# Kernel optimization log

Measured on AMD Instinct MI355X. Metric: run time of the kernel, lower is better.

The kernel has to match this reference:

```python
import jax, jax.numpy as jnp
import numpy as np

NEG_SLOPE = 0.2

def gat_conv(x, src, dst, W, a_src, a_dst, bias, num_nodes, heads, out_ch, concat):
    # x: [N, Fin]; W: [Fin, heads*out_ch]; a_src/a_dst: [heads, out_ch]
    h = (x @ W).reshape(num_nodes, heads, out_ch)            # [N,H,C]
    alpha_s = jnp.einsum('nhc,hc->nh', h, a_src)             # [N,H]
    alpha_d = jnp.einsum('nhc,hc->nh', h, a_dst)             # [N,H]
    e = alpha_s[src] + alpha_d[dst]                          # [E,H]
    e = jnp.where(e > 0, e, NEG_SLOPE * e)                   # LeakyReLU
    # segment softmax over incoming edges per destination node
    m = jax.ops.segment_max(e, dst, num_segments=num_nodes)  # [N,H]
    m = jnp.where(jnp.isfinite(m), m, 0.0)
    ee = jnp.exp(e - m[dst])                                 # [E,H]
    s = jax.ops.segment_sum(ee, dst, num_segments=num_nodes) # [N,H]
    alpha = ee / (s[dst] + 1e-16)                            # [E,H]
    out = jax.ops.segment_sum(h[src] * alpha[:, :, None], dst,
                              num_segments=num_nodes)        # [N,H,C]
    if concat:
        out = out.reshape(num_nodes, heads * out_ch)
    else:
        out = out.mean(axis=1)
    return out + bias


def setup_inputs() -> dict:
    key = jax.random.key(0)
    ks = jax.random.split(key, 10)
    N, E = 50000, 800000
    EMB, HID, HEADS, REPR = 128, 128, 8, 64
    C1 = HID // HEADS  # 16
    x = jax.random.normal(ks[0], (N, EMB), dtype=jnp.float32)
    edge_index = jax.random.randint(ks[1], (2, E), 0, N, dtype=jnp.int32)
    sc = 1.0 / np.sqrt(EMB)
    W1 = jax.random.normal(ks[2], (EMB, HEADS * C1), dtype=jnp.float32) * sc
    a1_src = jax.random.normal(ks[3], (HEADS, C1), dtype=jnp.float32) * 0.1
    a1_dst = jax.random.normal(ks[4], (HEADS, C1), dtype=jnp.float32) * 0.1
    b1 = jnp.zeros((HID,), dtype=jnp.float32)
    sc2 = 1.0 / np.sqrt(HID)
    W2 = jax.random.normal(ks[5], (HID, REPR), dtype=jnp.float32) * sc2
    a2_src = jax.random.normal(ks[6], (1, REPR), dtype=jnp.float32) * 0.1
    a2_dst = jax.random.normal(ks[7], (1, REPR), dtype=jnp.float32) * 0.1
    b2 = jnp.zeros((REPR,), dtype=jnp.float32)
    return {"x": x, "edge_index": edge_index,
            "W1": W1, "a1_src": a1_src, "a1_dst": a1_dst, "b1": b1,
            "W2": W2, "a2_src": a2_src, "a2_dst": a2_dst, "b2": b2}


def reference(x, edge_index, W1, a1_src, a1_dst, b1, W2, a2_src, a2_dst, b2):
    N = x.shape[0]
    # PyG GATConv adds self-loops by default
    loops = jnp.arange(N, dtype=edge_index.dtype)
    src = jnp.concatenate([edge_index[0], loops])
    dst = jnp.concatenate([edge_index[1], loops])
    # eval mode: F.dropout(p=0.6) is identity
    h = gat_conv(x, src, dst, W1, a1_src, a1_dst, b1, N,
                 heads=8, out_ch=16, concat=True)
    h = jax.nn.elu(h)
    out = gat_conv(h, src, dst, W2, a2_src, a2_dst, b2, N,
                   heads=1, out_ch=64, concat=True)
    return out
```

## Files before the change

### kernel.cpp

```cpp
#include <hip/hip_runtime.h>
#include <hip/hip_fp16.h>
#include <math.h>


typedef _Float16 f16x8 __attribute__((ext_vector_type(8)));
typedef float f32x4 __attribute__((ext_vector_type(4)));

#define NCHUNK 32
#define MAXBDIV 8192

__device__ __forceinline__ float leaky_exp(float e) {
    e = (e > 0.f) ? e : 0.2f * e;
    return __expf(e);
}

__device__ __forceinline__ void acc16(float w, float4 hv0, float4 hv1,
                                      float* __restrict__ acc) {
    const __half2* p0 = (const __half2*)&hv0;
    const __half2* p1 = (const __half2*)&hv1;
#pragma unroll
    for (int k = 0; k < 4; k++) {
        float2 f = __half22float2(p0[k]);
        acc[2 * k] += w * f.x;
        acc[2 * k + 1] += w * f.y;
    }
#pragma unroll
    for (int k = 0; k < 4; k++) {
        float2 f = __half22float2(p1[k]);
        acc[8 + 2 * k] += w * f.x;
        acc[8 + 2 * k + 1] += w * f.y;
    }
}

__device__ __forceinline__ void acc8(float w, float4 hv,
                                     float* __restrict__ acc) {
    const __half2* hp = (const __half2*)&hv;
#pragma unroll
    for (int k = 0; k < 4; k++) {
        float2 f = __half22float2(hp[k]);
        acc[2 * k] += w * f.x;
        acc[2 * k + 1] += w * f.y;
    }
}

__global__ __launch_bounds__(256) void augw_kernel(const float* __restrict__ W1,
                                                   const float* __restrict__ a1s,
                                                   const float* __restrict__ a1d,
                                                   const float* __restrict__ W2,
                                                   const float* __restrict__ a2s,
                                                   const float* __restrict__ a2d,
                                                   _Float16* __restrict__ W1t,
                                                   _Float16* __restrict__ W2t) {
    int t = threadIdx.x;
    if (blockIdx.x == 0) {
        for (int i = t; i < 144 * 128; i += 256) {
            int c = i >> 7, k = i & 127;
            float v;
            if (c < 128) {
                v = W1[k * 128 + c];
            } else if (c < 136) {
                int h = c - 128; v = 0.f;
#pragma unroll
                for (int j = 0; j < 16; j++) v += W1[k * 128 + h * 16 + j] * a1s[h * 16 + j];
            } else {
                int h = c - 136; v = 0.f;
#pragma unroll
                for (int j = 0; j < 16; j++) v += W1[k * 128 + h * 16 + j] * a1d[h * 16 + j];
            }
            W1t[c * 128 + k] = (_Float16)v;
        }
    } else {
        for (int i = t; i < 80 * 128; i += 256) {
            int c = i >> 7, k = i & 127;
            float v = 0.f;
            if (c < 64) {
                v = W2[k * 64 + c];
            } else if (c == 64) {
                for (int j = 0; j < 64; j++) v += W2[k * 64 + j] * a2s[j];
            } else if (c == 65) {
                for (int j = 0; j < 64; j++) v += W2[k * 64 + j] * a2d[j];
            }
            W2t[c * 128 + k] = (_Float16)v;
        }
    }
}

__global__ __launch_bounds__(256) void gemm1_bucket_kernel(
        const float* __restrict__ x, const _Float16* __restrict__ W1t,
        __half* __restrict__ h1, float* __restrict__ als,
        float* __restrict__ ald, int N, int gridG1,
        const int* __restrict__ src, const int* __restrict__ dst, int E,
        int* __restrict__ bucketCnt, int2* __restrict__ pairs) {
    __shared__ _Float16 Xs[64 * 136];
    int t = threadIdx.x;
    if ((int)blockIdx.x >= gridG1) {
        int* lcnt = (int*)Xs;
        int* lbase = lcnt + 8;
        if (t < 8) lcnt[t] = 0;
        __syncthreads();
        int bid = blockIdx.x - gridG1;
        int bdiv = (N + 7) >> 3;
        int i0 = (bid * 256 + t) * 4;
        int s_[4], d_[4], bk[4], rk[4];
        int nv = 0;
        if (i0 + 3 < E) {
            int4 d4 = *(const int4*)(dst + i0);
            int4 s4 = *(const int4*)(src + i0);
            s_[0] = s4.x; s_[1] = s4.y; s_[2] = s4.z; s_[3] = s4.w;
            d_[0] = d4.x; d_[1] = d4.y; d_[2] = d4.z; d_[3] = d4.w;
            nv = 4;
        } else {
            for (int k = i0; k < E && nv < 4; k++) {
                s_[nv] = src[k]; d_[nv] = dst[k]; nv++;
            }
        }
        int lane = t & 63;
        unsigned long long below = (lane == 0) ? 0ULL : (~0ULL >> (64 - lane));
#pragma unroll
        for (int u = 0; u < 4; u++) {
            bool v = (u < nv);
            int d = v ? d_[u] : 0;
            int b = d / bdiv;
            unsigned long long m0 = __ballot(b & 1);
            unsigned long long m1 = __ballot(b & 2);
            unsigned long long m2 = __ballot(b & 4);
            unsigned long long vm = __ballot(v);
            unsigned long long me = ((b & 1) ? m0 : ~m0) & ((b & 2) ? m1 : ~m1) &
                                    ((b & 4) ? m2 : ~m2) & vm;
            int leader = __ffsll((unsigned long long)me) - 1;
            int ldr = (leader < 0) ? 0 : leader;
            int cnt = __popcll(me);
            int rank = __popcll(me & below);
            int base = 0;
            if (v && lane == leader) base = atomicAdd(&lcnt[b], cnt);
            base = __shfl(base, ldr);
            bk[u] = b;
            rk[u] = base + rank;
        }
        __syncthreads();
        if (t < 8) lbase[t] = atomicAdd(&bucketCnt[t * 16], lcnt[t]);
        __syncthreads();
#pragma unroll 4
        for (int k = 0; k < nv; k++) {
            pairs[(size_t)bk[k] * E + lbase[bk[k]] + rk[k]] = make_int2(s_[k], d_[k]);
        }
        return;
    }
    int row0 = blockIdx.x * 64;
    for (int i = t; i < 2048; i += 256) {
        int r = i >> 5, c4 = i & 31;
        int gr = row0 + r;
        float4 v = make_float4(0.f, 0.f, 0.f, 0.f);
        if (gr < N) v = *(const float4*)(x + (size_t)gr * 128 + c4 * 4);
        _Float16* dp = Xs + r * 136 + c4 * 4;
        dp[0] = (_Float16)v.x; dp[1] = (_Float16)v.y;
        dp[2] = (_Float16)v.z; dp[3] = (_Float16)v.w;
    }
    __syncthreads();
    int w = t >> 6, L = t & 63, m = L & 15, quad = L >> 4;
    f32x4 acc[9];
#pragma unroll
    for (int f = 0; f < 9; f++) acc[f] = (f32x4){0.f, 0.f, 0.f, 0.f};
    const _Float16* Arow = Xs + (w * 16 + m) * 136 + quad * 8;
    const _Float16* Brow = W1t + m * 128 + quad * 8;
#pragma unroll
    for (int kt = 0; kt < 4; kt++) {
        f16x8 a = *(const f16x8*)(Arow + kt * 32);
#pragma unroll
        for (int f = 0; f < 9; f++) {
            f16x8 b = *(const f16x8*)(Brow + f * 2048 + kt * 32);
            acc[f] = __builtin_amdgcn_mfma_f32_16x16x32_f16(a, b, acc[f], 0, 0, 0);
        }
    }
    int nbase = row0 + w * 16 + quad * 4;
#pragma unroll
    for (int r = 0; r < 4; r++) {
        int n = nbase + r;
        if (n < N) {
            __half* hrow = h1 + (size_t)n * 128 + m;
#pragma unroll
            for (int f = 0; f < 8; f++) hrow[f * 16] = __float2half(acc[f][r]);
            float v = acc[8][r];
            if (m < 8) als[n * 8 + m] = v;
            else ald[n * 8 + (m - 8)] = v;
        }
    }
}

__global__ __launch_bounds__(256) void subhist_kernel(
        const int* __restrict__ bucketCnt, const int2* __restrict__ pairs,
        int E, int N, int* __restrict__ subcnt) {
    __shared__ int hist[MAXBDIV];
    int t = threadIdx.x;
    int b = blockIdx.x & 7;
    int j = blockIdx.x >> 3;
    int bdiv = (N + 7) >> 3;
    for (int i = t; i < bdiv; i += 256) hist[i] = 0;
    __syncthreads();
    int cnt = bucketCnt[b * 16];
    int chunk = (cnt + NCHUNK - 1) / NCHUNK;
    int lo = j * chunk;
    int hi = min(lo + chunk, cnt);
    const int2* plist = pairs + (size_t)b * E;
    int blo = b * bdiv;
    for (int i = lo + t; i < hi; i += 256) {
        int d = plist[i].y;
        atomicAdd(&hist[d - blo], 1);
    }
    __syncthreads();
    int* out = subcnt + (size_t)(b * NCHUNK + j) * bdiv;
    for (int i = t; i < bdiv; i += 256) out[i] = hist[i];
}

__global__ __launch_bounds__(256) void scan1_kernel(const int* __restrict__ subcnt,
                                                    int N,
                                                    int* __restrict__ rowstart,
                                                    int* __restrict__ blocksum) {
    __shared__ int tmp[256];
    int t = threadIdx.x;
    int i = blockIdx.x * 256 + t;
    int bdiv = (N + 7) >> 3;
    int v = 0;
    if (i < N) {
        int b = i / bdiv;
        int local = i - b * bdiv;
        const int* sc = subcnt + (size_t)b * NCHUNK * bdiv + local;
#pragma unroll
        for (int j = 0; j < NCHUNK; j++) v += sc[(size_t)j * bdiv];
    }
    tmp[t] = v;
    __syncthreads();
    for (int off = 1; off < 256; off <<= 1) {
        int x = (t >= off) ? tmp[t - off] : 0;
        __syncthreads();
        tmp[t] += x;
        __syncthreads();
    }
    if (i < N) rowstart[i] = tmp[t] - v;
    if (t == 255) blocksum[blockIdx.x] = tmp[t];
}

__global__ __launch_bounds__(256) void scan23_kernel(int* __restrict__ rowstart,
                                                     const int* __restrict__ blocksum,
                                                     int nb,
                                                     int* __restrict__ subcnt,
                                                     int N, int E) {
    __shared__ int sdata[256];
    int t = threadIdx.x;
    int bx = blockIdx.x;
    sdata[t] = (t < nb && t < bx) ? blocksum[t] : 0;
    __syncthreads();
#pragma unroll
    for (int off = 128; off > 0; off >>= 1) {
        if (t < off) sdata[t] += sdata[t + off];
        __syncthreads();
    }
    int offset = sdata[0];
    int i = bx * 256 + t;
    int bdiv = (N + 7) >> 3;
    if (i < N) {
        int v = rowstart[i] + offset;
        rowstart[i] = v;
        int b = i / bdiv;
        int local = i - b * bdiv;
        int* sc = subcnt + (size_t)b * NCHUNK * bdiv + local;
        int c = v;
#pragma unroll
        for (int j = 0; j < NCHUNK; j++) {
            int cj = sc[(size_t)j * bdiv];
            sc[(size_t)j * bdiv] = c;
            c += cj;
        }
    } else if (i == N) {
        rowstart[N] = E;
    }
}

__global__ __launch_bounds__(256) void scatter_kernel(
        const int* __restrict__ bucketCnt, const int2* __restrict__ pairs,
        int E, int N, const int* __restrict__ subcnt, int* __restrict__ esrc) {
    __shared__ int lcur[MAXBDIV];
    int t = threadIdx.x;
    int b = blockIdx.x & 7;
    int j = blockIdx.x >> 3;
    int bdiv = (N + 7) >> 3;
    const int* base = subcnt + (size_t)(b * NCHUNK + j) * bdiv;
    for (int i = t; i < bdiv; i += 256) lcur[i] = base[i];
    __syncthreads();
    int cnt = bucketCnt[b * 16];
    int chunk = (cnt + NCHUNK - 1) / NCHUNK;
    int lo = j * chunk;
    int hi = min(lo + chunk, cnt);
    const int2* plist = pairs + (size_t)b * E;
    int blo = b * bdiv;
    for (int i = lo + t; i < hi; i += 256) {
        int2 p = plist[i];
        int pos = atomicAdd(&lcur[p.y - blo], 1);
        esrc[pos] = p.x;
    }
}

__global__ __launch_bounds__(256) void agg1_kernel(const __half* __restrict__ h1,
                                                   const float* __restrict__ als,
                                                   const float* __restrict__ ald,
                                                   const int* __restrict__ rowstart,
                                                   const int* __restrict__ esrc,
                                                   const float* __restrict__ b1,
                                                   __half* __restrict__ act1, int N) {
    int t = threadIdx.x;
    int lane = t & 63;
    int grp = lane >> 3;
    int q = lane & 7;
    int bdiv = (N + 7) >> 3;
    int ln = (blockIdx.x >> 3) * 32 + (t >> 6) * 8 + grp;
    if (ln >= bdiv) return;
    int n = (blockIdx.x & 7) * bdiv + ln;
    if (n >= N) return;
    const float4* h1v = (const float4*)h1;
    float adv = ald[n * 8 + q];
    float acc[16];
#pragma unroll
    for (int k = 0; k < 16; k++) acc[k] = 0.f;
    float wsum = 0.f;
    {
        float w = leaky_exp(als[n * 8 + q] + adv);
        wsum += w;
        acc16(w, h1v[(size_t)n * 16 + 2 * q], h1v[(size_t)n * 16 + 2 * q + 1], acc);
    }
    int beg = rowstart[n], end = rowstart[n + 1];
    int j = beg;
    for (; j + 4 <= end; j += 4) {
        int s0 = esrc[j], s1 = esrc[j + 1], s2 = esrc[j + 2], s3 = esrc[j + 3];
        float4 a0 = h1v[(size_t)s0 * 16 + 2 * q], b0 = h1v[(size_t)s0 * 16 + 2 * q + 1];
        float4 a1 = h1v[(size_t)s1 * 16 + 2 * q], b1 = h1v[(size_t)s1 * 16 + 2 * q + 1];
        float4 a2 = h1v[(size_t)s2 * 16 + 2 * q], b2 = h1v[(size_t)s2 * 16 + 2 * q + 1];
        float4 a3 = h1v[(size_t)s3 * 16 + 2 * q], b3 = h1v[(size_t)s3 * 16 + 2 * q + 1];
        float e0 = als[s0 * 8 + q], e1 = als[s1 * 8 + q];
        float e2 = als[s2 * 8 + q], e3 = als[s3 * 8 + q];
        float w0 = leaky_exp(e0 + adv), w1 = leaky_exp(e1 + adv);
        float w2 = leaky_exp(e2 + adv), w3 = leaky_exp(e3 + adv);
        wsum += (w0 + w1) + (w2 + w3);
        acc16(w0, a0, b0, acc);
        acc16(w1, a1, b1, acc);
        acc16(w2, a2, b2, acc);
        acc16(w3, a3, b3, acc);
    }
    for (; j < end; j++) {
        int s = esrc[j];
        float w = leaky_exp(als[s * 8 + q] + adv);
        wsum += w;
        acc16(w, h1v[(size_t)s * 16 + 2 * q], h1v[(size_t)s * 16 + 2 * q + 1], acc);
    }
    float inv = 1.f / (wsum + 1e-16f);
    const float* bf = b1 + q * 16;
    __align__(16) __half2 po[8];
#pragma unroll
    for (int k = 0; k < 8; k++) {
        float o0 = acc[2 * k] * inv + bf[2 * k];
        float o1 = acc[2 * k + 1] * inv + bf[2 * k + 1];
        o0 = (o0 > 0.f) ? o0 : (__expf(o0) - 1.f);
        o1 = (o1 > 0.f) ? o1 : (__expf(o1) - 1.f);
        po[k] = __floats2half2_rn(o0, o1);
    }
    float4* ov = (float4*)(act1 + (size_t)n * 128 + q * 16);
    ov[0] = ((float4*)po)[0];
    ov[1] = ((float4*)po)[1];
}

__global__ __launch_bounds__(256) void gemm2_kernel(const __half* __restrict__ act1,
                                                    const _Float16* __restrict__ W2t,
                                                    __half* __restrict__ h2,
                                                    float* __restrict__ al2s,
                                                    float* __restrict__ al2d, int N) {
    int t = threadIdx.x;
    int row0 = blockIdx.x * 64;
    int w = t >> 6, L = t & 63, m = L & 15, quad = L >> 4;
    f32x4 acc[5];
#pragma unroll
    for (int f = 0; f < 5; f++) acc[f] = (f32x4){0.f, 0.f, 0.f, 0.f};
    const _Float16* Arow =
        (const _Float16*)act1 + (size_t)(row0 + w * 16 + m) * 128 + quad * 8;
    const _Float16* Brow = W2t + m * 128 + quad * 8;
#pragma unroll
    for (int kt = 0; kt < 4; kt++) {
        f16x8 a = *(const f16x8*)(Arow + kt * 32);
#pragma unroll
        for (int f = 0; f < 5; f++) {
            f16x8 b = *(const f16x8*)(Brow + f * 2048 + kt * 32);
            acc[f] = __builtin_amdgcn_mfma_f32_16x16x32_f16(a, b, acc[f], 0, 0, 0);
        }
    }
    int nbase = row0 + w * 16 + quad * 4;
#pragma unroll
    for (int r = 0; r < 4; r++) {
        int n = nbase + r;
        if (n < N) {
            __half* hrow = h2 + (size_t)n * 64 + m;
#pragma unroll
            for (int f = 0; f < 4; f++) hrow[f * 16] = __float2half(acc[f][r]);
            if (m == 0) al2s[n] = acc[4][r];
            else if (m == 1) al2d[n] = acc[4][r];
        }
    }
}

__global__ __launch_bounds__(256) void agg2_kernel(const __half* __restrict__ h2,
                                                   const float* __restrict__ al2s,
                                                   const float* __restrict__ al2d,
                                                   const int* __restrict__ rowstart,
                                                   const int* __restrict__ esrc,
                                                   const float* __restrict__ b2,
                                                   float* __restrict__ out, int N) {
    int t = threadIdx.x;
    int lane = t & 63;
    int grp = lane >> 3;
    int q = lane & 7;
    int bdiv = (N + 7) >> 3;
    int ln = (blockIdx.x >> 3) * 32 + (t >> 6) * 8 + grp;
    if (ln >= bdiv) return;
    int n = (blockIdx.x & 7) * bdiv + ln;
    if (n >= N) return;
    const float4* h2v = (const float4*)h2;
    float adv = al2d[n];
    float acc[8];
#pragma unroll
    for (int k = 0; k < 8; k++) acc[k] = 0.f;
    float wsum = 0.f;
    {
        float w = leaky_exp(al2s[n] + adv);
        wsum += w;
        acc8(w, h2v[(size_t)n * 8 + q], acc);
    }
    int beg = rowstart[n], end = rowstart[n + 1];
    int j = beg;
    for (; j + 4 <= end; j += 4) {
        int s0 = esrc[j], s1 = esrc[j + 1], s2 = esrc[j + 2], s3 = esrc[j + 3];
        float4 a0 = h2v[(size_t)s0 * 8 + q];
        float4 a1 = h2v[(size_t)s1 * 8 + q];
        float4 a2 = h2v[(size_t)s2 * 8 + q];
        float4 a3 = h2v[(size_t)s3 * 8 + q];
        float e0 = al2s[s0], e1 = al2s[s1], e2 = al2s[s2], e3 = al2s[s3];
        float w0 = leaky_exp(e0 + adv), w1 = leaky_exp(e1 + adv);
        float w2 = leaky_exp(e2 + adv), w3 = leaky_exp(e3 + adv);
        wsum += (w0 + w1) + (w2 + w3);
        acc8(w0, a0, acc);
        acc8(w1, a1, acc);
        acc8(w2, a2, acc);
        acc8(w3, a3, acc);
    }
    for (; j < end; j++) {
        int s = esrc[j];
        float w = leaky_exp(al2s[s] + adv);
        wsum += w;
        acc8(w, h2v[(size_t)s * 8 + q], acc);
    }
    float inv = 1.f / (wsum + 1e-16f);
    const float* bf = b2 + q * 8;
    float4* ov = (float4*)(out + (size_t)n * 64 + q * 8);
    ov[0] = make_float4(acc[0] * inv + bf[0], acc[1] * inv + bf[1],
                        acc[2] * inv + bf[2], acc[3] * inv + bf[3]);
    ov[1] = make_float4(acc[4] * inv + bf[4], acc[5] * inv + bf[5],
                        acc[6] * inv + bf[6], acc[7] * inv + bf[7]);
}

extern "C" void kernel_launch(void* const* d_in, const int* in_sizes, int n_in,
                              void* d_out, int out_size, void* d_ws, size_t ws_size,
                              hipStream_t stream) {
    (void)n_in; (void)out_size; (void)ws_size;
    const float* x   = (const float*)d_in[0];
    const int*   ei  = (const int*)d_in[1];
    const float* W1  = (const float*)d_in[2];
    const float* a1s = (const float*)d_in[3];
    const float* a1d = (const float*)d_in[4];
    const float* b1  = (const float*)d_in[5];
    const float* W2  = (const float*)d_in[6];
    const float* a2s = (const float*)d_in[7];
    const float* a2d = (const float*)d_in[8];
    const float* b2  = (const float*)d_in[9];
    float* out = (float*)d_out;

    const int N = in_sizes[0] / 128;
    const int E = in_sizes[1] / 2;
    const int* src = ei;
    const int* dst = ei + E;
    const int bdiv = (N + 7) / 8;

    char* wp = (char*)d_ws;
    auto alloc = [&](size_t bytes) -> void* {
        void* p = (void*)wp;
        wp += (bytes + 255) & ~(size_t)255;
        return p;
    };
    __half* h1   = (__half*)alloc((size_t)N * 128 * 2);
    __half* act1 = (__half*)alloc((size_t)N * 128 * 2);
    __half* h2   = (__half*)alloc((size_t)N * 64 * 2 + 64 * 256);
    float* al1s = (float*)alloc((size_t)N * 8 * 4);
    float* al1d = (float*)alloc((size_t)N * 8 * 4);
    float* al2s = (float*)alloc((size_t)N * 4);
    float* al2d = (float*)alloc((size_t)N * 4);
    int* bucketCnt = (int*)alloc(8 * 16 * 4);
    int* subcnt   = (int*)alloc((size_t)8 * NCHUNK * bdiv * 4);
    int* rowstart = (int*)alloc((size_t)(N + 1) * 4);
    int* esrc     = (int*)alloc((size_t)E * 4);
    int2* pairs   = (int2*)alloc((size_t)8 * E * 8);
    int* blocksum = (int*)alloc(256 * 4);
    _Float16* W1t = (_Float16*)alloc(144 * 128 * 2);
    _Float16* W2t = (_Float16*)alloc(80 * 128 * 2);

    const int nbScan = (N + 255) / 256;
    const int gridH  = (E + 1023) / 1024;
    const int gridG1 = (N + 63) / 64;
    const int gridG2 = (N + 63) / 64;
    const int gridAggN = 8 * ((bdiv + 31) / 32);
    const int gridSort = 8 * NCHUNK;

    hipMemsetAsync(bucketCnt, 0, 8 * 16 * 4, stream);

    augw_kernel<<<2, 256, 0, stream>>>(W1, a1s, a1d, W2, a2s, a2d, W1t, W2t);
    gemm1_bucket_kernel<<<gridG1 + gridH, 256, 0, stream>>>(
        x, W1t, h1, al1s, al1d, N, gridG1, src, dst, E, bucketCnt, pairs);
    subhist_kernel<<<gridSort, 256, 0, stream>>>(bucketCnt, pairs, E, N, subcnt);
    scan1_kernel<<<nbScan, 256, 0, stream>>>(subcnt, N, rowstart, blocksum);
    scan23_kernel<<<(N + 256) / 256, 256, 0, stream>>>(rowstart, blocksum, nbScan,
                                                       subcnt, N, E);
    scatter_kernel<<<gridSort, 256, 0, stream>>>(bucketCnt, pairs, E, N, subcnt, esrc);

    agg1_kernel<<<gridAggN, 256, 0, stream>>>(h1, al1s, al1d, rowstart, esrc, b1, act1, N);
    gemm2_kernel<<<gridG2, 256, 0, stream>>>(act1, W2t, h2, al2s, al2d, N);
    agg2_kernel<<<gridAggN, 256, 0, stream>>>(h2, al2s, al2d, rowstart, esrc, b2, out, N);
}
```

Baseline: 232.9 us.

## Fuse layer-1 aggregation with layer-2 GEMM and pack edge pairs into 32 bits

Layer-1 aggregation and the second projection GEMM now run as one kernel. Each block writes its 32 ELU-activated rows into shared memory and runs MFMA on them directly, so the act1 intermediate buffer and one kernel launch go away. Bucketed edge pairs are packed as a 16-bit local destination plus a 16-bit source index in one 32-bit word. This halves the pair traffic in the bucket, histogram and scatter passes. The packing silently assumes fewer than 65536 nodes, and the fused GEMM runs on 32-row tiles with uneven work across waves.

```diff
diff --git a/kernel.cpp b/kernel.cpp
--- a/kernel.cpp
+++ b/kernel.cpp
@@ -90,7 +90,7 @@
         __half* __restrict__ h1, float* __restrict__ als,
         float* __restrict__ ald, int N, int gridG1,
         const int* __restrict__ src, const int* __restrict__ dst, int E,
-        int* __restrict__ bucketCnt, int2* __restrict__ pairs) {
+        int* __restrict__ bucketCnt, unsigned* __restrict__ pairs) {
     __shared__ _Float16 Xs[64 * 136];
     int t = threadIdx.x;
     if ((int)blockIdx.x >= gridG1) {
@@ -142,7 +142,9 @@
         __syncthreads();
 #pragma unroll 4
         for (int k = 0; k < nv; k++) {
-            pairs[(size_t)bk[k] * E + lbase[bk[k]] + rk[k]] = make_int2(s_[k], d_[k]);
+            unsigned dlocal = (unsigned)(d_[k] - bk[k] * ((N + 7) >> 3));
+            pairs[(size_t)bk[k] * E + lbase[bk[k]] + rk[k]] =
+                (dlocal << 16) | (unsigned)s_[k];
         }
         return;
     }
@@ -188,7 +190,7 @@
 }
 
 __global__ __launch_bounds__(256) void subhist_kernel(
-        const int* __restrict__ bucketCnt, const int2* __restrict__ pairs,
+        const int* __restrict__ bucketCnt, const unsigned* __restrict__ pairs,
         int E, int N, int* __restrict__ subcnt) {
     __shared__ int hist[MAXBDIV];
     int t = threadIdx.x;
@@ -201,11 +203,9 @@
     int chunk = (cnt + NCHUNK - 1) / NCHUNK;
     int lo = j * chunk;
     int hi = min(lo + chunk, cnt);
-    const int2* plist = pairs + (size_t)b * E;
-    int blo = b * bdiv;
+    const unsigned* plist = pairs + (size_t)b * E;
     for (int i = lo + t; i < hi; i += 256) {
-        int d = plist[i].y;
-        atomicAdd(&hist[d - blo], 1);
+        atomicAdd(&hist[plist[i] >> 16], 1);
     }
     __syncthreads();
     int* out = subcnt + (size_t)(b * NCHUNK + j) * bdiv;
@@ -277,7 +277,7 @@
 }
 
 __global__ __launch_bounds__(256) void scatter_kernel(
-        const int* __restrict__ bucketCnt, const int2* __restrict__ pairs,
+        const int* __restrict__ bucketCnt, const unsigned* __restrict__ pairs,
         int E, int N, const int* __restrict__ subcnt, int* __restrict__ esrc) {
     __shared__ int lcur[MAXBDIV];
     int t = threadIdx.x;
@@ -291,48 +291,50 @@
     int chunk = (cnt + NCHUNK - 1) / NCHUNK;
     int lo = j * chunk;
     int hi = min(lo + chunk, cnt);
-    const int2* plist = pairs + (size_t)b * E;
-    int blo = b * bdiv;
+    const unsigned* plist = pairs + (size_t)b * E;
     for (int i = lo + t; i < hi; i += 256) {
-        int2 p = plist[i];
-        int pos = atomicAdd(&lcur[p.y - blo], 1);
-        esrc[pos] = p.x;
-    }
-}
-
-__global__ __launch_bounds__(256) void agg1_kernel(const __half* __restrict__ h1,
-                                                   const float* __restrict__ als,
-                                                   const float* __restrict__ ald,
-                                                   const int* __restrict__ rowstart,
-                                                   const int* __restrict__ esrc,
-                                                   const float* __restrict__ b1,
-                                                   __half* __restrict__ act1, int N) {
+        unsigned p = plist[i];
+        int pos = atomicAdd(&lcur[p >> 16], 1);
+        esrc[pos] = (int)(p & 0xFFFFu);
+    }
+}
+
+__global__ __launch_bounds__(256) void agg1_gemm2_kernel(
+        const __half* __restrict__ h1, const float* __restrict__ als,
+        const float* __restrict__ ald, const int* __restrict__ rowstart,
+        const int* __restrict__ esrc, const float* __restrict__ b1,
+        const _Float16* __restrict__ W2t, __half* __restrict__ h2,
+        float* __restrict__ al2s, float* __restrict__ al2d, int N) {
+    __shared__ _Float16 actS[32 * 136];
     int t = threadIdx.x;
     int lane = t & 63;
     int grp = lane >> 3;
     int q = lane & 7;
     int bdiv = (N + 7) >> 3;
-    int ln = (blockIdx.x >> 3) * 32 + (t >> 6) * 8 + grp;
-    if (ln >= bdiv) return;
+    int lrow = (t >> 6) * 8 + grp;
+    int ln = (blockIdx.x >> 3) * 32 + lrow;
     int n = (blockIdx.x & 7) * bdiv + ln;
-    if (n >= N) return;
+    bool valid = (ln < bdiv) && (n < N);
     const float4* h1v = (const float4*)h1;
-    float adv = ald[n * 8 + q];
     float acc[16];
 #pragma unroll
     for (int k = 0; k < 16; k++) acc[k] = 0.f;
     float wsum = 0.f;
-    {
-        float w = leaky_exp(als[n * 8 + q] + adv);
-        wsum += w;
-        acc16(w, h1v[(size_t)n * 16 + 2 * q], h1v[(size_t)n * 16 + 2 * q + 1], acc);
-    }
-    int beg = rowstart[n], end = rowstart[n + 1];
+    int beg = 0, end = 0;
+    float adv = 0.f;
+    if (valid) {
+        adv = ald[n * 8 + q];
+        float wself = leaky_exp(als[n * 8 + q] + adv);
+        wsum = wself;
+        acc16(wself, h1v[(size_t)n * 16 + 2 * q], h1v[(size_t)n * 16 + 2 * q + 1], acc);
+        beg = rowstart[n];
+        end = rowstart[n + 1];
+    }
     int j = beg;
     for (; j + 4 <= end; j += 4) {
         int s0 = esrc[j], s1 = esrc[j + 1], s2 = esrc[j + 2], s3 = esrc[j + 3];
         float4 a0 = h1v[(size_t)s0 * 16 + 2 * q], b0 = h1v[(size_t)s0 * 16 + 2 * q + 1];
-        float4 a1 = h1v[(size_t)s1 * 16 + 2 * q], b1 = h1v[(size_t)s1 * 16 + 2 * q + 1];
+        float4 a1 = h1v[(size_t)s1 * 16 + 2 * q], b1v = h1v[(size_t)s1 * 16 + 2 * q + 1];
         float4 a2 = h1v[(size_t)s2 * 16 + 2 * q], b2 = h1v[(size_t)s2 * 16 + 2 * q + 1];
         float4 a3 = h1v[(size_t)s3 * 16 + 2 * q], b3 = h1v[(size_t)s3 * 16 + 2 * q + 1];
         float e0 = als[s0 * 8 + q], e1 = als[s1 * 8 + q];
@@ -341,7 +343,7 @@
         float w2 = leaky_exp(e2 + adv), w3 = leaky_exp(e3 + adv);
         wsum += (w0 + w1) + (w2 + w3);
         acc16(w0, a0, b0, acc);
-        acc16(w1, a1, b1, acc);
+        acc16(w1, a1, b1v, acc);
         acc16(w2, a2, b2, acc);
         acc16(w3, a3, b3, acc);
     }
@@ -351,55 +353,63 @@
         wsum += w;
         acc16(w, h1v[(size_t)s * 16 + 2 * q], h1v[(size_t)s * 16 + 2 * q + 1], acc);
     }
-    float inv = 1.f / (wsum + 1e-16f);
-    const float* bf = b1 + q * 16;
     __align__(16) __half2 po[8];
-#pragma unroll
-    for (int k = 0; k < 8; k++) {
-        float o0 = acc[2 * k] * inv + bf[2 * k];
-        float o1 = acc[2 * k + 1] * inv + bf[2 * k + 1];
-        o0 = (o0 > 0.f) ? o0 : (__expf(o0) - 1.f);
-        o1 = (o1 > 0.f) ? o1 : (__expf(o1) - 1.f);
-        po[k] = __floats2half2_rn(o0, o1);
-    }
-    float4* ov = (float4*)(act1 + (size_t)n * 128 + q * 16);
-    ov[0] = ((float4*)po)[0];
-    ov[1] = ((float4*)po)[1];
-}
-
-__global__ __launch_bounds__(256) void gemm2_kernel(const __half* __restrict__ act1,
-                                                    const _Float16* __restrict__ W2t,
-                                                    __half* __restrict__ h2,
-                                                    float* __restrict__ al2s,
-                                                    float* __restrict__ al2d, int N) {
-    int t = threadIdx.x;
-    int row0 = blockIdx.x * 64;
-    int w = t >> 6, L = t & 63, m = L & 15, quad = L >> 4;
-    f32x4 acc[5];
-#pragma unroll
-    for (int f = 0; f < 5; f++) acc[f] = (f32x4){0.f, 0.f, 0.f, 0.f};
-    const _Float16* Arow =
-        (const _Float16*)act1 + (size_t)(row0 + w * 16 + m) * 128 + quad * 8;
-    const _Float16* Brow = W2t + m * 128 + quad * 8;
+    if (valid) {
+        float inv = 1.f / (wsum + 1e-16f);
+        const float* bf = b1 + q * 16;
+#pragma unroll
+        for (int k = 0; k < 8; k++) {
+            float o0 = acc[2 * k] * inv + bf[2 * k];
+            float o1 = acc[2 * k + 1] * inv + bf[2 * k + 1];
+            o0 = (o0 > 0.f) ? o0 : (__expf(o0) - 1.f);
+            o1 = (o1 > 0.f) ? o1 : (__expf(o1) - 1.f);
+            po[k] = __floats2half2_rn(o0, o1);
+        }
+    } else {
+#pragma unroll
+        for (int k = 0; k < 8; k++) po[k] = __floats2half2_rn(0.f, 0.f);
+    }
+    *(float4*)(actS + lrow * 136 + q * 16) = ((float4*)po)[0];
+    *(float4*)(actS + lrow * 136 + q * 16 + 8) = ((float4*)po)[1];
+    __syncthreads();
+    int w4 = t >> 6;
+    int m = lane & 15, quad = lane >> 4;
+    int rt = w4 & 1;
+    int ctbase = (w4 < 2) ? 0 : 1;
+    f32x4 acc2[3];
+#pragma unroll
+    for (int f = 0; f < 3; f++) acc2[f] = (f32x4){0.f, 0.f, 0.f, 0.f};
+    const _Float16* Arow2 = actS + (rt * 16 + m) * 136 + quad * 8;
+    const _Float16* Brow2 = W2t + m * 128 + quad * 8;
 #pragma unroll
     for (int kt = 0; kt < 4; kt++) {
-        f16x8 a = *(const f16x8*)(Arow + kt * 32);
-#pragma unroll
-        for (int f = 0; f < 5; f++) {
-            f16x8 b = *(const f16x8*)(Brow + f * 2048 + kt * 32);
-            acc[f] = __builtin_amdgcn_mfma_f32_16x16x32_f16(a, b, acc[f], 0, 0, 0);
-        }
-    }
-    int nbase = row0 + w * 16 + quad * 4;
+        f16x8 a = *(const f16x8*)(Arow2 + kt * 32);
+#pragma unroll
+        for (int f = 0; f < 3; f++) {
+            int ctf = ctbase + 2 * f;
+            if (ctf < 5) {
+                f16x8 bb = *(const f16x8*)(Brow2 + ctf * 2048 + kt * 32);
+                acc2[f] = __builtin_amdgcn_mfma_f32_16x16x32_f16(a, bb, acc2[f], 0, 0, 0);
+            }
+        }
+    }
+    int secbase = (blockIdx.x & 7) * bdiv;
+    int lnbase = (blockIdx.x >> 3) * 32 + rt * 16 + quad * 4;
 #pragma unroll
     for (int r = 0; r < 4; r++) {
-        int n = nbase + r;
-        if (n < N) {
-            __half* hrow = h2 + (size_t)n * 64 + m;
-#pragma unroll
-            for (int f = 0; f < 4; f++) hrow[f * 16] = __float2half(acc[f][r]);
-            if (m == 0) al2s[n] = acc[4][r];
-            else if (m == 1) al2d[n] = acc[4][r];
+        int ln2 = lnbase + r;
+        int n2 = secbase + ln2;
+        if (ln2 < bdiv && n2 < N) {
+#pragma unroll
+            for (int f = 0; f < 3; f++) {
+                int ctf = ctbase + 2 * f;
+                if (ctf < 4) {
+                    h2[(size_t)n2 * 64 + ctf * 16 + m] = __float2half(acc2[f][r]);
+                } else if (ctf == 4) {
+                    if (m == 0) al2s[n2] = acc2[f][r];
+                    else if (m == 1) al2d[n2] = acc2[f][r];
+                }
+            }
         }
     }
 }
@@ -492,7 +502,6 @@
         return p;
     };
     __half* h1   = (__half*)alloc((size_t)N * 128 * 2);
-    __half* act1 = (__half*)alloc((size_t)N * 128 * 2);
     __half* h2   = (__half*)alloc((size_t)N * 64 * 2 + 64 * 256);
     float* al1s = (float*)alloc((size_t)N * 8 * 4);
     float* al1d = (float*)alloc((size_t)N * 8 * 4);
@@ -502,7 +511,7 @@
     int* subcnt   = (int*)alloc((size_t)8 * NCHUNK * bdiv * 4);
     int* rowstart = (int*)alloc((size_t)(N + 1) * 4);
     int* esrc     = (int*)alloc((size_t)E * 4);
-    int2* pairs   = (int2*)alloc((size_t)8 * E * 8);
+    unsigned* pairs = (unsigned*)alloc((size_t)8 * E * 4);
     int* blocksum = (int*)alloc(256 * 4);
     _Float16* W1t = (_Float16*)alloc(144 * 128 * 2);
     _Float16* W2t = (_Float16*)alloc(80 * 128 * 2);
@@ -510,7 +519,6 @@
     const int nbScan = (N + 255) / 256;
     const int gridH  = (E + 1023) / 1024;
     const int gridG1 = (N + 63) / 64;
-    const int gridG2 = (N + 63) / 64;
     const int gridAggN = 8 * ((bdiv + 31) / 32);
     const int gridSort = 8 * NCHUNK;
 
@@ -525,7 +533,7 @@
                                                        subcnt, N, E);
     scatter_kernel<<<gridSort, 256, 0, stream>>>(bucketCnt, pairs, E, N, subcnt, esrc);
 
-    agg1_kernel<<<gridAggN, 256, 0, stream>>>(h1, al1s, al1d, rowstart, esrc, b1, act1, N);
-    gemm2_kernel<<<gridG2, 256, 0, stream>>>(act1, W2t, h2, al2s, al2d, N);
+    agg1_gemm2_kernel<<<gridAggN, 256, 0, stream>>>(h1, al1s, al1d, rowstart, esrc,
+                                                    b1, W2t, h2, al2s, al2d, N);
     agg2_kernel<<<gridAggN, 256, 0, stream>>>(h2, al2s, al2d, rowstart, esrc, b2, out, N);
 }
```

Result: faster. 220.8 us (-5.2%).
